# Performance work log

Hardware: AMD Instinct MI355X
Metric: run time of the kernel (lower is better)

The kernel has to match this reference:

```python
import jax, jax.numpy as jnp
import numpy as np

IN_F = 2048
OUT_F = 2048
N_ROWS = 8192


def _perm(n):
    # t_o(n) is a permutation matrix P with P[i, p(i)] = 1, p(i) = (4i mod n) + (4i // n)
    i = np.arange(n)
    return (4 * i) % n + (4 * i) // n


def _inv(p):
    inv = np.empty_like(p)
    inv[p] = np.arange(len(p))
    return inv

# (P_in^T @ H)[a, :] = H[i, :] where p_in(i) = a  ->  rows indexed by inv(p_in)
_INV_P_IN = _inv(_perm(IN_F))
# (H @ P_out)[:, b] = H[:, j] where p_out(j) = b  ->  cols indexed by inv(p_out)
_INV_P_OUT = _inv(_perm(OUT_F))


def make_quaternion_mul(kernel):
    # kernel: (in//4, out); split along dim 1 into quaternion components
    r, i, j, k = jnp.split(kernel, 4, axis=1)
    r2 = jnp.concatenate([r, -i, -j, -k], axis=1)
    i2 = jnp.concatenate([i, r, -k, j], axis=1)
    j2 = jnp.concatenate([j, k, r, -i], axis=1)
    k2 = jnp.concatenate([k, -j, i, r], axis=1)
    return jnp.concatenate([r2, i2, j2, k2], axis=0)  # (in, out)


def setup_inputs() -> dict:
    key = jax.random.key(0)
    k1, k2, k3 = jax.random.split(key, 3)
    inp = jax.random.normal(k1, (N_ROWS, IN_F), dtype=jnp.float32)
    weight = jax.random.normal(k2, (IN_F // 4, OUT_F), dtype=jnp.float32) * (1.0 / np.sqrt(IN_F // 4))
    bias = jax.random.normal(k3, (OUT_F,), dtype=jnp.float32) * 0.01
    return {"input": inp, "weight": weight, "bias": bias}


def reference(input, weight, bias):
    hamilton = make_quaternion_mul(weight)                 # (in, out)
    # swap=True: hamilton = L^T @ hamilton @ R, both pure permutations
    hamilton = hamilton[_INV_P_IN][:, _INV_P_OUT]
    support = input @ hamilton + bias[None, :]             # (N, out)
    return support
```

## Files before the change

### kernel.cpp

```cpp
#include <hip/hip_runtime.h>
#include <stdint.h>

#define IN_F 2048
#define OUT_F 2048
#define N_ROWS 8192

#define BM 256
#define BN 256
#define BK 32
#define NT (IN_F / BK)
#define TM_TILES (N_ROWS / BM)
#define TN_TILES (OUT_F / BN)
#define NWG (TM_TILES * TN_TILES)
#define TILE_SHORTS (BM * BK)
#define BUF_SHORTS (2 * TILE_SHORTS)

typedef __bf16 bf16x8 __attribute__((ext_vector_type(8)));
typedef float f32x4 __attribute__((ext_vector_type(4)));
typedef unsigned short ushortx8 __attribute__((ext_vector_type(8)));

__device__ __forceinline__ unsigned short f2bf(float f) {
  unsigned u = __builtin_bit_cast(unsigned, f);
  u += 0x7FFFu + ((u >> 16) & 1u);
  return (unsigned short)(u >> 16);
}

__device__ __forceinline__ void async16(void* lds, const void* g) {
  __builtin_amdgcn_global_load_lds(
      (const __attribute__((address_space(1))) void*)(uintptr_t)g,
      (__attribute__((address_space(3))) void*)(uint32_t)(uintptr_t)lds,
      16, 0, 0);
}

__global__ __launch_bounds__(256) void k_convertA(const float* __restrict__ A,
                                                  unsigned short* __restrict__ Ab) {
  const size_t t = (size_t)blockIdx.x * 256 + threadIdx.x;
  const float4* a4 = reinterpret_cast<const float4*>(A);
  float4 v0 = a4[2 * t];
  float4 v1 = a4[2 * t + 1];
  ushortx8 o;
  o[0] = f2bf(v0.x); o[1] = f2bf(v0.y); o[2] = f2bf(v0.z); o[3] = f2bf(v0.w);
  o[4] = f2bf(v1.x); o[5] = f2bf(v1.y); o[6] = f2bf(v1.z); o[7] = f2bf(v1.w);
  *reinterpret_cast<ushortx8*>(Ab + t * 8) = o;
}

__global__ __launch_bounds__(256) void k_buildHt(const float* __restrict__ W,
                                                 unsigned short* __restrict__ Ht) {
  const int t = blockIdx.x * 256 + threadIdx.x;
  const int b = t >> 8;
  const int a0 = (t & 255) << 3;
  const int c = b & 3, v = b >> 2;
  ushortx8 o;
#pragma unroll
  for (int e = 0; e < 8; ++e) {
    const int a = a0 + e;
    const int q = a & 3, u = a >> 2;
    float w = W[(size_t)u * OUT_F + ((q ^ c) << 9) + v];
    if ((0x284E >> ((q << 2) | c)) & 1) w = -w;
    o[e] = f2bf(w);
  }
  *reinterpret_cast<ushortx8*>(Ht + (size_t)b * IN_F + a0) = o;
}

__global__ __launch_bounds__(512, 2) void k_gemm(const unsigned short* __restrict__ A,
                                                 const unsigned short* __restrict__ Bt,
                                                 const float* __restrict__ bias,
                                                 float* __restrict__ C) {
  __shared__ __align__(16) unsigned short lds[4 * BUF_SHORTS];

  const int tid = threadIdx.x;
  const int lane = tid & 63;
  const int w = tid >> 6;
  const int wm = w >> 2;
  const int wn = w & 3;
  const int fr = lane & 15;
  const int g = lane >> 4;

  const int wg = blockIdx.x;
  const int swz = (wg & 7) * (NWG >> 3) + (wg >> 3);
  const int tm = swz >> 3;
  const int tn = swz & 7;
  const int row0 = tm * BM, col0 = tn * BN;

  const unsigned short* srcA[2];
  const unsigned short* srcB[2];
  int tOff[2];
#pragma unroll
  for (int i = 0; i < 2; ++i) {
    const int t = w * 128 + i * 64 + lane;
    const int r = t >> 2, s = t & 3;
    const int ga = s ^ ((r >> 1) & 3);
    srcA[i] = A + (size_t)(row0 + r) * IN_F + ga * 8;
    srcB[i] = Bt + (size_t)(col0 + r) * IN_F + ga * 8;
    tOff[i] = t * 8;
  }

#define STAGE(T)                                              \
  do {                                                        \
    unsigned short* base_ = &lds[((T) & 3) * BUF_SHORTS];     \
    const int ko_ = (T) * BK;                                 \
    async16(base_ + tOff[0], srcA[0] + ko_);                  \
    async16(base_ + tOff[1], srcA[1] + ko_);                  \
    async16(base_ + TILE_SHORTS + tOff[0], srcB[0] + ko_);    \
    async16(base_ + TILE_SHORTS + tOff[1], srcB[1] + ko_);    \
  } while (0)

  int offA[8], offB[4];
#pragma unroll
  for (int m = 0; m < 8; ++m) {
    const int r = wm * 128 + m * 16 + fr;
    offA[m] = r * BK + (g ^ ((r >> 1) & 3)) * 8;
  }
#pragma unroll
  for (int n = 0; n < 4; ++n) {
    const int r = wn * 64 + n * 16 + fr;
    offB[n] = r * BK + (g ^ ((r >> 1) & 3)) * 8;
  }

  f32x4 acc[8][4] = {};

  STAGE(0);
  STAGE(1);
  STAGE(2);

#define TILE(T, VMSTR, DOSTAGE)                                               \
  do {                                                                        \
    asm volatile("s_waitcnt vmcnt(" VMSTR ")" ::: "memory");                  \
    __builtin_amdgcn_s_barrier();                                             \
    __builtin_amdgcn_sched_barrier(0);                                        \
    const unsigned short* ab_ = &lds[((T) & 3) * BUF_SHORTS];                 \
    const unsigned short* bb_ = ab_ + TILE_SHORTS;                            \
    bf16x8 af[8], bg[4];                                                      \
    _Pragma("unroll") for (int m = 0; m < 8; ++m)                             \
        af[m] = __builtin_bit_cast(                                           \
            bf16x8, *reinterpret_cast<const ushortx8*>(ab_ + offA[m]));       \
    _Pragma("unroll") for (int n = 0; n < 4; ++n)                             \
        bg[n] = __builtin_bit_cast(                                           \
            bf16x8, *reinterpret_cast<const ushortx8*>(bb_ + offB[n]));       \
    if (DOSTAGE) STAGE((T) + 3);                                              \
    __builtin_amdgcn_s_setprio(1);                                            \
    _Pragma("unroll") for (int m = 0; m < 8; ++m)                             \
        _Pragma("unroll") for (int n = 0; n < 4; ++n)                         \
            acc[m][n] = __builtin_amdgcn_mfma_f32_16x16x32_bf16(              \
                af[m], bg[n], acc[m][n], 0, 0, 0);                            \
    __builtin_amdgcn_s_setprio(0);                                            \
  } while (0)

  for (int t = 0; t < NT - 3; ++t) {
    TILE(t, "8", true);
  }
  TILE(NT - 3, "8", false);
  TILE(NT - 2, "4", false);
  TILE(NT - 1, "0", false);

#undef TILE
#undef STAGE

  const int g4 = g << 2;
  float bv[4];
#pragma unroll
  for (int n = 0; n < 4; ++n) bv[n] = bias[col0 + wn * 64 + n * 16 + fr];
#pragma unroll
  for (int m = 0; m < 8; ++m) {
#pragma unroll
    for (int e = 0; e < 4; ++e) {
      const int row = row0 + wm * 128 + m * 16 + g4 + e;
      float* cp = C + (size_t)row * OUT_F + col0 + wn * 64 + fr;
#pragma unroll
      for (int n = 0; n < 4; ++n) cp[n * 16] = acc[m][n][e] + bv[n];
    }
  }
}

__global__ __launch_bounds__(256) void k_naive(const float* __restrict__ A,
                                               const float* __restrict__ W,
                                               const float* __restrict__ bias,
                                               float* __restrict__ C) {
  const int idx = blockIdx.x * 256 + threadIdx.x;
  const int m = idx >> 11;
  const int b = idx & (OUT_F - 1);
  const int c = b & 3, v = b >> 2;
  float acc = 0.f;
  const float* arow = A + (size_t)m * IN_F;
  for (int a = 0; a < IN_F; ++a) {
    const int q = a & 3, u = a >> 2;
    float h = W[(size_t)u * OUT_F + ((q ^ c) << 9) + v];
    if ((0x284E >> ((q << 2) | c)) & 1) h = -h;
    acc += arow[a] * h;
  }
  C[idx] = acc + bias[b];
}

extern "C" void kernel_launch(void* const* d_in, const int* in_sizes, int n_in,
                              void* d_out, int out_size, void* d_ws, size_t ws_size,
                              hipStream_t stream) {
  (void)in_sizes; (void)n_in; (void)out_size;
  const float* inp  = (const float*)d_in[0];
  const float* w    = (const float*)d_in[1];
  const float* bias = (const float*)d_in[2];
  float* out = (float*)d_out;

  const size_t needA = (size_t)N_ROWS * IN_F * sizeof(unsigned short);
  const size_t needH = (size_t)IN_F * OUT_F * sizeof(unsigned short);
  if (ws_size < needA + needH) {
    k_naive<<<(N_ROWS * OUT_F) / 256, 256, 0, stream>>>(inp, w, bias, out);
    return;
  }

  unsigned short* Ab = (unsigned short*)d_ws;
  unsigned short* Ht = Ab + (size_t)N_ROWS * IN_F;

  k_convertA<<<(N_ROWS * IN_F) / (8 * 256), 256, 0, stream>>>(inp, Ab);
  k_buildHt<<<(IN_F * OUT_F) / (8 * 256), 256, 0, stream>>>(w, Ht);
  k_gemm<<<NWG, 512, 0, stream>>>(Ab, Ht, bias, out);
}
```

Before: 101.6 us.

## Pre-tile bf16 operands into LDS-ready swizzled blocks and fuse prep kernels

The conversion kernels now write A and the Hamilton matrix in a tiled, pre-swizzled layout: each 256x32 tile sits contiguously in exactly the order the GEMM's LDS expects. The GEMM stage loads then become contiguous 16-byte copies with simple offsets instead of strided row reads. The two prep kernels are merged into one launch to save a launch and its tail. The cost is a more complex prep indexing scheme, and the prep kernel's global writes are scattered differently than before.

```diff
diff --git a/kernel.cpp b/kernel.cpp
--- a/kernel.cpp
+++ b/kernel.cpp
@@ -32,38 +32,53 @@
       16, 0, 0);
 }
 
-__global__ __launch_bounds__(256) void k_convertA(const float* __restrict__ A,
-                                                  unsigned short* __restrict__ Ab) {
-  const size_t t = (size_t)blockIdx.x * 256 + threadIdx.x;
-  const float4* a4 = reinterpret_cast<const float4*>(A);
-  float4 v0 = a4[2 * t];
-  float4 v1 = a4[2 * t + 1];
-  ushortx8 o;
-  o[0] = f2bf(v0.x); o[1] = f2bf(v0.y); o[2] = f2bf(v0.z); o[3] = f2bf(v0.w);
-  o[4] = f2bf(v1.x); o[5] = f2bf(v1.y); o[6] = f2bf(v1.z); o[7] = f2bf(v1.w);
-  *reinterpret_cast<ushortx8*>(Ab + t * 8) = o;
-}
-
-__global__ __launch_bounds__(256) void k_buildHt(const float* __restrict__ W,
-                                                 unsigned short* __restrict__ Ht) {
-  const int t = blockIdx.x * 256 + threadIdx.x;
-  const int b = t >> 8;
-  const int a0 = (t & 255) << 3;
-  const int c = b & 3, v = b >> 2;
-  ushortx8 o;
-#pragma unroll
-  for (int e = 0; e < 8; ++e) {
-    const int a = a0 + e;
-    const int q = a & 3, u = a >> 2;
-    float w = W[(size_t)u * OUT_F + ((q ^ c) << 9) + v];
-    if ((0x284E >> ((q << 2) | c)) & 1) w = -w;
-    o[e] = f2bf(w);
-  }
-  *reinterpret_cast<ushortx8*>(Ht + (size_t)b * IN_F + a0) = o;
-}
-
-__global__ __launch_bounds__(512, 2) void k_gemm(const unsigned short* __restrict__ A,
-                                                 const unsigned short* __restrict__ Bt,
+__device__ __forceinline__ bf16x8 ld8(const unsigned short* p) {
+  return __builtin_bit_cast(bf16x8, *reinterpret_cast<const ushortx8*>(p));
+}
+
+__global__ __launch_bounds__(256) void k_prep(const float* __restrict__ A,
+                                              unsigned short* __restrict__ AbT,
+                                              const float* __restrict__ W,
+                                              unsigned short* __restrict__ BtT) {
+  const int bid = blockIdx.x;
+  if (bid < 8192) {
+    const int tile = bid >> 2;
+    const int t = ((bid & 3) << 8) + threadIdx.x;
+    const int r = t >> 2;
+    const int ga = (t & 3) ^ ((r >> 1) & 3);
+    const int R = tile >> 6, T = tile & 63;
+    const float* src = A + (size_t)(R * 256 + r) * IN_F + T * 32 + ga * 8;
+    const float4 v0 = *reinterpret_cast<const float4*>(src);
+    const float4 v1 = *reinterpret_cast<const float4*>(src + 4);
+    ushortx8 o;
+    o[0] = f2bf(v0.x); o[1] = f2bf(v0.y); o[2] = f2bf(v0.z); o[3] = f2bf(v0.w);
+    o[4] = f2bf(v1.x); o[5] = f2bf(v1.y); o[6] = f2bf(v1.z); o[7] = f2bf(v1.w);
+    *reinterpret_cast<ushortx8*>(AbT + (size_t)tile * 8192 + t * 8) = o;
+  } else {
+    const int bb = bid - 8192;
+    const int tile = bb >> 2;
+    const int t = ((bb & 3) << 8) + threadIdx.x;
+    const int r = t >> 2;
+    const int ga = (t & 3) ^ ((r >> 1) & 3);
+    const int Ct = tile >> 6, T = tile & 63;
+    const int b = Ct * 256 + r;
+    const int c = b & 3, v = b >> 2;
+    const int a0 = T * 32 + ga * 8;
+    ushortx8 o;
+#pragma unroll
+    for (int e = 0; e < 8; ++e) {
+      const int a = a0 + e;
+      const int q = a & 3, u = a >> 2;
+      float w = W[(size_t)u * OUT_F + ((q ^ c) << 9) + v];
+      if ((0x284E >> ((q << 2) | c)) & 1) w = -w;
+      o[e] = f2bf(w);
+    }
+    *reinterpret_cast<ushortx8*>(BtT + (size_t)tile * 8192 + t * 8) = o;
+  }
+}
+
+__global__ __launch_bounds__(512, 2) void k_gemm(const unsigned short* __restrict__ AbT,
+                                                 const unsigned short* __restrict__ BtT,
                                                  const float* __restrict__ bias,
                                                  float* __restrict__ C) {
   __shared__ __align__(16) unsigned short lds[4 * BUF_SHORTS];
@@ -82,42 +97,37 @@
   const int tn = swz & 7;
   const int row0 = tm * BM, col0 = tn * BN;
 
-  const unsigned short* srcA[2];
-  const unsigned short* srcB[2];
-  int tOff[2];
-#pragma unroll
-  for (int i = 0; i < 2; ++i) {
-    const int t = w * 128 + i * 64 + lane;
-    const int r = t >> 2, s = t & 3;
-    const int ga = s ^ ((r >> 1) & 3);
-    srcA[i] = A + (size_t)(row0 + r) * IN_F + ga * 8;
-    srcB[i] = Bt + (size_t)(col0 + r) * IN_F + ga * 8;
-    tOff[i] = t * 8;
-  }
-
-#define STAGE(T)                                              \
-  do {                                                        \
-    unsigned short* base_ = &lds[((T) & 3) * BUF_SHORTS];     \
-    const int ko_ = (T) * BK;                                 \
-    async16(base_ + tOff[0], srcA[0] + ko_);                  \
-    async16(base_ + tOff[1], srcA[1] + ko_);                  \
-    async16(base_ + TILE_SHORTS + tOff[0], srcB[0] + ko_);    \
-    async16(base_ + TILE_SHORTS + tOff[1], srcB[1] + ko_);    \
+  const unsigned short* baseA = AbT + (size_t)tm * 64 * 8192;
+  const unsigned short* baseB = BtT + (size_t)tn * 64 * 8192;
+  const int tOff0 = (w * 128 + lane) * 8;
+  const int tOff1 = (w * 128 + 64 + lane) * 8;
+
+#define STAGE(T)                                                   \
+  do {                                                             \
+    unsigned short* base_ = &lds[((T) & 3) * BUF_SHORTS];          \
+    const unsigned short* sa_ = baseA + (size_t)(T) * 8192;        \
+    const unsigned short* sb_ = baseB + (size_t)(T) * 8192;        \
+    async16(base_ + tOff0, sa_ + tOff0);                           \
+    async16(base_ + tOff1, sa_ + tOff1);                           \
+    async16(base_ + TILE_SHORTS + tOff0, sb_ + tOff0);             \
+    async16(base_ + TILE_SHORTS + tOff1, sb_ + tOff1);             \
   } while (0)
 
   int offA[8], offB[4];
 #pragma unroll
   for (int m = 0; m < 8; ++m) {
     const int r = wm * 128 + m * 16 + fr;
-    offA[m] = r * BK + (g ^ ((r >> 1) & 3)) * 8;
+    offA[m] = r * BK + ((g ^ ((r >> 1) & 3)) << 3);
   }
 #pragma unroll
   for (int n = 0; n < 4; ++n) {
     const int r = wn * 64 + n * 16 + fr;
-    offB[n] = r * BK + (g ^ ((r >> 1) & 3)) * 8;
+    offB[n] = TILE_SHORTS + r * BK + ((g ^ ((r >> 1) & 3)) << 3);
   }
 
   f32x4 acc[8][4] = {};
+
+#define MFMA_(a_, b_, c_) __builtin_amdgcn_mfma_f32_16x16x32_bf16(a_, b_, c_, 0, 0, 0)
 
   STAGE(0);
   STAGE(1);
@@ -128,21 +138,15 @@
     asm volatile("s_waitcnt vmcnt(" VMSTR ")" ::: "memory");                  \
     __builtin_amdgcn_s_barrier();                                             \
     __builtin_amdgcn_sched_barrier(0);                                        \
-    const unsigned short* ab_ = &lds[((T) & 3) * BUF_SHORTS];                 \
-    const unsigned short* bb_ = ab_ + TILE_SHORTS;                            \
-    bf16x8 af[8], bg[4];                                                      \
-    _Pragma("unroll") for (int m = 0; m < 8; ++m)                             \
-        af[m] = __builtin_bit_cast(                                           \
-            bf16x8, *reinterpret_cast<const ushortx8*>(ab_ + offA[m]));       \
-    _Pragma("unroll") for (int n = 0; n < 4; ++n)                             \
-        bg[n] = __builtin_bit_cast(                                           \
-            bf16x8, *reinterpret_cast<const ushortx8*>(bb_ + offB[n]));       \
+    const unsigned short* b_ = &lds[((T) & 3) * BUF_SHORTS];                  \
+    bf16x8 bg[4], af[8];                                                      \
+    _Pragma("unroll") for (int n = 0; n < 4; ++n) bg[n] = ld8(b_ + offB[n]);  \
+    _Pragma("unroll") for (int m = 0; m < 8; ++m) af[m] = ld8(b_ + offA[m]);  \
     if (DOSTAGE) STAGE((T) + 3);                                              \
     __builtin_amdgcn_s_setprio(1);                                            \
     _Pragma("unroll") for (int m = 0; m < 8; ++m)                             \
-        _Pragma("unroll") for (int n = 0; n < 4; ++n)                         \
-            acc[m][n] = __builtin_amdgcn_mfma_f32_16x16x32_bf16(              \
-                af[m], bg[n], acc[m][n], 0, 0, 0);                            \
+      _Pragma("unroll") for (int n = 0; n < 4; ++n)                           \
+        acc[m][n] = MFMA_(af[m], bg[n], acc[m][n]);                           \
     __builtin_amdgcn_s_setprio(0);                                            \
   } while (0)
 
@@ -207,10 +211,9 @@
     return;
   }
 
-  unsigned short* Ab = (unsigned short*)d_ws;
-  unsigned short* Ht = Ab + (size_t)N_ROWS * IN_F;
-
-  k_convertA<<<(N_ROWS * IN_F) / (8 * 256), 256, 0, stream>>>(inp, Ab);
-  k_buildHt<<<(IN_F * OUT_F) / (8 * 256), 256, 0, stream>>>(w, Ht);
-  k_gemm<<<NWG, 512, 0, stream>>>(Ab, Ht, bias, out);
-}
+  unsigned short* AbT = (unsigned short*)d_ws;
+  unsigned short* BtT = AbT + (size_t)N_ROWS * IN_F;
+
+  k_prep<<<8192 + 2048, 256, 0, stream>>>(inp, AbT, w, BtT);
+  k_gemm<<<NWG, 512, 0, stream>>>(AbT, BtT, bias, out);
+}
```

New measurement: 86.67 us. 1.17x faster.
